# Optimization experiments

Hardware: AMD Instinct MI355X
Metric: run time of the kernel (lower is better)

## Reference

```python
import jax, jax.numpy as jnp
import numpy as np

N_NODES = 100000   # number of graph nodes
N_EDGES = 1600000  # adjacency nnz (avg degree 16)
FEAT_NNZ = 1600000 # sparse feature nnz (~16 per node)
F_IN = 512
F_OUT = 128


def setup_inputs() -> dict:
    key = jax.random.key(0)
    k1, k2, k3, k4, k5, k6 = jax.random.split(key, 6)
    adj_indices = jax.random.randint(k1, (2, N_EDGES), 0, N_NODES, dtype=jnp.int64 if jax.config.jax_enable_x64 else jnp.int32)
    adj_values = jax.random.uniform(k2, (N_EDGES,), dtype=jnp.float32)
    feat_rows = jax.random.randint(k3, (FEAT_NNZ,), 0, N_NODES)
    feat_cols = jax.random.randint(k4, (FEAT_NNZ,), 0, F_IN)
    feat_values = jax.random.uniform(k5, (FEAT_NNZ,), dtype=jnp.float32)
    # xavier_uniform init of the dense weight, as in the torch module
    bound = float(np.sqrt(6.0 / (F_IN + F_OUT)))
    weight = jax.random.uniform(k6, (F_IN, F_OUT), dtype=jnp.float32, minval=-bound, maxval=bound)
    return {
        "adj_indices": adj_indices,
        "adj_values": adj_values,
        "feat_rows": feat_rows,
        "feat_cols": feat_cols,
        "feat_values": feat_values,
        "weight": weight,
        "num_nodes": N_NODES,
    }


def _spmm(rows, cols, vals, num_rows, dense):
    """COO sparse [num_rows, ?] @ dense [?, K] -> [num_rows, K]."""
    msgs = vals[:, None] * dense[cols]          # [nnz, K] gather + scale
    return jax.ops.segment_sum(msgs, rows, num_segments=num_rows)


def reference(adj_indices, adj_values, feat_rows, feat_cols, feat_values, weight, num_nodes):
    # spmm(features, W): sparse [N, F_in] @ [F_in, F_out]
    base_features = _spmm(feat_rows, feat_cols, feat_values, num_nodes, weight)
    # spmm(A_hat, base): sparse [N, N] @ [N, F_out]  -- neighbor aggregation
    out = _spmm(adj_indices[0], adj_indices[1], adj_values, num_nodes, base_features)
    return out
```

## Files before the change

kernel.cpp:

```cpp
#include <hip/hip_runtime.h>
#include <stdint.h>

#define N_NODES 100000
#define F_IN    512
#define F_OUT   128
#define BROWS   128
#define NBKT    ((N_NODES + BROWS - 1) / BROWS)
#define CAP     2560
#define EPB     4096

typedef unsigned short     u16;
typedef unsigned int       u32;
typedef unsigned long long u64;
typedef long long          i64;

__device__ __forceinline__ float b2f(u16 u) {
    union { u32 i; float f; } x; x.i = ((u32)u) << 16; return x.f;
}
__device__ __forceinline__ u16 f2b(float f) {
    u32 i = __float_as_uint(f);
    return (u16)((i + 0x7fffu + ((i >> 16) & 1u)) >> 16);
}
__device__ __forceinline__ float blo(u32 u) { return __uint_as_float(u << 16); }
__device__ __forceinline__ float bhi(u32 u) { return __uint_as_float(u & 0xFFFF0000u); }
__device__ __forceinline__ int ld_idx(const void* p, int i, int w64) {
    return w64 ? (int)((const i64*)p)[i] : ((const int*)p)[i];
}
__device__ __forceinline__ u16 ld_val_bf(const void* p, int i, int f32) {
    return f32 ? f2b(((const float*)p)[i]) : ((const u16*)p)[i];
}

__device__ __forceinline__ void ld_idx4(int* r, const void* p, int g, int w64) {
    if (w64) {
        const i64* q = (const i64*)p + 4 * (size_t)g;
        longlong2 a = *(const longlong2*)q;
        longlong2 b = *(const longlong2*)(q + 2);
        r[0] = (int)a.x; r[1] = (int)a.y; r[2] = (int)b.x; r[3] = (int)b.y;
    } else {
        int4 a = *(const int4*)((const int*)p + 4 * (size_t)g);
        r[0] = a.x; r[1] = a.y; r[2] = a.z; r[3] = a.w;
    }
}
__device__ __forceinline__ void ld_val4(u32* v, const void* p, int g, int f32) {
    if (f32) {
        float4 a = *(const float4*)((const float*)p + 4 * (size_t)g);
        v[0] = f2b(a.x); v[1] = f2b(a.y); v[2] = f2b(a.z); v[3] = f2b(a.w);
    } else {
        ushort4 a = *(const ushort4*)((const u16*)p + 4 * (size_t)g);
        v[0] = a.x; v[1] = a.y; v[2] = a.z; v[3] = a.w;
    }
}

__device__ __forceinline__ void sniff3(const u16* w, const u32* adj, const u32* frows,
                                       int* sf, int t) {
    if (t < 64) {
        u32 e0 = (w[t]      >> 7) & 0xFF;
        u32 e1 = (w[64 + t] >> 7) & 0xFF;
        u64 bad = __ballot((e0 > 0x7B) || (e1 > 0x7B));
        u64 za = __ballot(adj[2 * t + 1] == 0u);
        u64 zf = __ballot(frows[2 * t + 1] == 0u);
        if (t == 0) {
            sf[0] = (bad != 0);
            sf[1] = (__popcll(za) >= 32);
            sf[2] = (__popcll(zf) >= 32);
        }
    }
}

__global__ __launch_bounds__(512, 4) void binF_k(
        const void* __restrict__ frows, const void* __restrict__ fcols,
        const void* __restrict__ fvals, int M,
        const void* __restrict__ adjbase, const u16* __restrict__ weight,
        int* __restrict__ gcurF, u32* __restrict__ fbkt) {
    __shared__ int hist[NBKT];
    __shared__ int hbase[NBKT];
    __shared__ int sf[3];
    int t = threadIdx.x;
    sniff3(weight, (const u32*)adjbase, (const u32*)frows, sf, t);
    for (int i = t; i < NBKT; i += 512) hist[i] = 0;
    __syncthreads();
    int f32 = sf[0], f64 = sf[2];
    int start = blockIdx.x * EPB;
    int end = min(start + EPB, M);
    int r[8]; int c[8]; u32 v[8];
    #pragma unroll
    for (int h = 0; h < 2; ++h) {
        int g = (start >> 2) + t + h * 512;
        int e0 = 4 * g;
        if (e0 + 3 < end) {
            ld_idx4(r + 4 * h, frows, g, f64);
            ld_idx4(c + 4 * h, fcols, g, f64);
            ld_val4(v + 4 * h, fvals, g, f32);
        } else {
            #pragma unroll
            for (int j = 0; j < 4; ++j) {
                int jj = 4 * h + j;
                if (e0 + j < end) {
                    r[jj] = ld_idx(frows, e0 + j, f64);
                    c[jj] = ld_idx(fcols, e0 + j, f64);
                    v[jj] = ld_val_bf(fvals, e0 + j, f32);
                } else r[jj] = -1;
            }
        }
    }
    #pragma unroll
    for (int j = 0; j < 8; ++j) if (r[j] >= 0) atomicAdd(&hist[r[j] >> 7], 1);
    __syncthreads();
    for (int i = t; i < NBKT; i += 512) {
        int h = hist[i];
        hbase[i] = h ? atomicAdd(&gcurF[i], h) : 0;
        hist[i] = 0;
    }
    __syncthreads();
    #pragma unroll
    for (int j = 0; j < 8; ++j) if (r[j] >= 0) {
        int b = r[j] >> 7;
        int pos = hbase[b] + atomicAdd(&hist[b], 1);
        if (pos < CAP)
            fbkt[(size_t)b * CAP + pos] = (v[j] << 16) | ((u32)(r[j] & 127) << 9) | (u32)c[j];
    }
}

union S1Mem {
    struct { int hist[NBKT]; int hbase[NBKT]; } bin;
    struct { u32 csr[CAP]; int hcnt[BROWS]; int roff[BROWS + 1]; int cur[BROWS]; } s1;
};

__global__ __launch_bounds__(512, 4) void binAs1_k(
        const void* __restrict__ adjbase, const void* __restrict__ avals, int E, int nAb,
        const u32* __restrict__ frsn, const u16* __restrict__ weight,
        int* __restrict__ gcurA, u64* __restrict__ abkt,
        const int* __restrict__ cntF, const u32* __restrict__ fbkt,
        const void* __restrict__ W, u16* __restrict__ base) {
    __shared__ S1Mem sm;
    __shared__ int sf[3];
    int t = threadIdx.x;
    sniff3(weight, (const u32*)adjbase, frsn, sf, t);
    if ((int)blockIdx.x < nAb) {
        for (int i = t; i < NBKT; i += 512) sm.bin.hist[i] = 0;
        __syncthreads();
        int f32 = sf[0], a64 = sf[1];
        const void* acols = a64 ? (const void*)((const i64*)adjbase + E)
                                : (const void*)((const int*)adjbase + E);
        int start = blockIdx.x * EPB;
        int end = min(start + EPB, E);
        int r[8]; int c[8]; u32 v[8];
        #pragma unroll
        for (int h = 0; h < 2; ++h) {
            int g = (start >> 2) + t + h * 512;
            int e0 = 4 * g;
            if (e0 + 3 < end) {
                ld_idx4(r + 4 * h, adjbase, g, a64);
                ld_idx4(c + 4 * h, acols, g, a64);
                ld_val4(v + 4 * h, avals, g, f32);
            } else {
                #pragma unroll
                for (int j = 0; j < 4; ++j) {
                    int jj = 4 * h + j;
                    if (e0 + j < end) {
                        r[jj] = ld_idx(adjbase, e0 + j, a64);
                        c[jj] = ld_idx(acols, e0 + j, a64);
                        v[jj] = ld_val_bf(avals, e0 + j, f32);
                    } else r[jj] = -1;
                }
            }
        }
        #pragma unroll
        for (int j = 0; j < 8; ++j) if (r[j] >= 0) atomicAdd(&sm.bin.hist[r[j] >> 7], 1);
        __syncthreads();
        for (int i = t; i < NBKT; i += 512) {
            int h = sm.bin.hist[i];
            sm.bin.hbase[i] = h ? atomicAdd(&gcurA[i], h) : 0;
            sm.bin.hist[i] = 0;
        }
        __syncthreads();
        #pragma unroll
        for (int j = 0; j < 8; ++j) if (r[j] >= 0) {
            int b = r[j] >> 7;
            int pos = sm.bin.hbase[b] + atomicAdd(&sm.bin.hist[b], 1);
            if (pos < CAP)
                abkt[(size_t)b * CAP + pos] =
                    ((u64)v[j] << 24) | ((u64)(r[j] & 127) << 17) | (u64)(u32)c[j];
        }
        return;
    }
    int b = blockIdx.x - nAb;
    int n = cntF[b]; if (n > CAP) n = CAP;
    const u32* ed = fbkt + (size_t)b * CAP;
    if (t < BROWS) sm.s1.hcnt[t] = 0;
    __syncthreads();
    int f32 = sf[0];
    u32 pb[5];
    #pragma unroll
    for (int k = 0; k < 5; ++k) { int i = t + k * 512; pb[k] = (i < n) ? ed[i] : 0u; }
    #pragma unroll
    for (int k = 0; k < 5; ++k) { int i = t + k * 512; if (i < n) atomicAdd(&sm.s1.hcnt[(pb[k] >> 9) & 127], 1); }
    __syncthreads();
    if (t < 64) {
        int h0 = sm.s1.hcnt[2 * t], h1 = sm.s1.hcnt[2 * t + 1];
        int s = h0 + h1, v2 = s;
        #pragma unroll
        for (int off = 1; off < 64; off <<= 1) {
            int u = __shfl_up(v2, off);
            if (t >= off) v2 += u;
        }
        int excl = v2 - s;
        sm.s1.roff[2 * t] = excl;     sm.s1.roff[2 * t + 1] = excl + h0;
        sm.s1.cur[2 * t]  = excl;     sm.s1.cur[2 * t + 1]  = excl + h0;
        if (t == 63) sm.s1.roff[128] = v2;
    }
    __syncthreads();
    #pragma unroll
    for (int k = 0; k < 5; ++k) {
        int i = t + k * 512;
        if (i < n) {
            u32 p = pb[k];
            int pos = atomicAdd(&sm.s1.cur[(p >> 9) & 127], 1);
            sm.s1.csr[pos] = p;
        }
    }
    __syncthreads();
    int wave = t >> 6, lane = t & 63, g16 = lane >> 4, l16 = lane & 15;
    #pragma unroll
    for (int set = 0; set < 4; ++set) {
        int row = set * 32 + wave * 4 + g16;
        int s = sm.s1.roff[row], e = sm.s1.roff[row + 1];
        float a0 = 0.f, a1 = 0.f, a2 = 0.f, a3 = 0.f, a4 = 0.f, a5 = 0.f, a6 = 0.f, a7 = 0.f;
        if (f32) {
            const float* Wf = (const float*)W;
            for (int j0 = s; j0 < e; j0 += 4) {
                u32 p[4]; float4 qa[4], qb[4];
                #pragma unroll
                for (int k = 0; k < 4; ++k) { int jk = j0 + k; p[k] = sm.s1.csr[jk < e ? jk : e - 1]; }
                #pragma unroll
                for (int k = 0; k < 4; ++k) {
                    const float* wp = Wf + (size_t)(p[k] & 0x1FF) * F_OUT + l16 * 8;
                    qa[k] = *(const float4*)wp;
                    qb[k] = *(const float4*)(wp + 4);
                }
                #pragma unroll
                for (int k = 0; k < 4; ++k) {
                    float v = (j0 + k < e) ? b2f((u16)(p[k] >> 16)) : 0.f;
                    a0 += v * qa[k].x; a1 += v * qa[k].y;
                    a2 += v * qa[k].z; a3 += v * qa[k].w;
                    a4 += v * qb[k].x; a5 += v * qb[k].y;
                    a6 += v * qb[k].z; a7 += v * qb[k].w;
                }
            }
        } else {
            const u16* Wb = (const u16*)W;
            for (int j0 = s; j0 < e; j0 += 8) {
                u32 p[8]; uint4 q[8];
                #pragma unroll
                for (int k = 0; k < 8; ++k) { int jk = j0 + k; p[k] = sm.s1.csr[jk < e ? jk : e - 1]; }
                #pragma unroll
                for (int k = 0; k < 8; ++k)
                    q[k] = *(const uint4*)(Wb + (size_t)(p[k] & 0x1FF) * F_OUT + l16 * 8);
                #pragma unroll
                for (int k = 0; k < 8; ++k) {
                    float v = (j0 + k < e) ? b2f((u16)(p[k] >> 16)) : 0.f;
                    a0 += v * blo(q[k].x); a1 += v * bhi(q[k].x);
                    a2 += v * blo(q[k].y); a3 += v * bhi(q[k].y);
                    a4 += v * blo(q[k].z); a5 += v * bhi(q[k].z);
                    a6 += v * blo(q[k].w); a7 += v * bhi(q[k].w);
                }
            }
        }
        int gr = b * BROWS + row;
        if (gr < N_NODES) {
            uint4 o;
            o.x = (u32)f2b(a0) | ((u32)f2b(a1) << 16);
            o.y = (u32)f2b(a2) | ((u32)f2b(a3) << 16);
            o.z = (u32)f2b(a4) | ((u32)f2b(a5) << 16);
            o.w = (u32)f2b(a6) | ((u32)f2b(a7) << 16);
            *(uint4*)(base + (size_t)gr * F_OUT + l16 * 8) = o;
        }
    }
}

__global__ __launch_bounds__(512, 4) void stage2_k(const int* __restrict__ cnt,
        const u64* __restrict__ bkts, const u16* __restrict__ base,
        const void* __restrict__ W, const u32* __restrict__ adjsn,
        const u32* __restrict__ frsn, void* __restrict__ out) {
    __shared__ u64 csr[CAP];
    __shared__ int hcnt[BROWS];
    __shared__ int roff[BROWS + 1];
    __shared__ int cur[BROWS];
    __shared__ int sf[3];
    int t = threadIdx.x;
    sniff3((const u16*)W, adjsn, frsn, sf, t);
    int b = blockIdx.x;
    int n = cnt[b]; if (n > CAP) n = CAP;
    const u64* ed = bkts + (size_t)b * CAP;
    if (t < BROWS) hcnt[t] = 0;
    __syncthreads();
    u64 pb[5];
    #pragma unroll
    for (int k = 0; k < 5; ++k) { int i = t + k * 512; pb[k] = (i < n) ? ed[i] : 0ull; }
    #pragma unroll
    for (int k = 0; k < 5; ++k) { int i = t + k * 512; if (i < n) atomicAdd(&hcnt[(int)((pb[k] >> 17) & 127)], 1); }
    __syncthreads();
    if (t < 64) {
        int h0 = hcnt[2 * t], h1 = hcnt[2 * t + 1];
        int s = h0 + h1, v2 = s;
        #pragma unroll
        for (int off = 1; off < 64; off <<= 1) {
            int u = __shfl_up(v2, off);
            if (t >= off) v2 += u;
        }
        int excl = v2 - s;
        roff[2 * t] = excl;     roff[2 * t + 1] = excl + h0;
        cur[2 * t]  = excl;     cur[2 * t + 1]  = excl + h0;
        if (t == 63) roff[128] = v2;
    }
    __syncthreads();
    #pragma unroll
    for (int k = 0; k < 5; ++k) {
        int i = t + k * 512;
        if (i < n) {
            u64 p = pb[k];
            int pos = atomicAdd(&cur[(int)((p >> 17) & 127)], 1);
            csr[pos] = p;
        }
    }
    __syncthreads();
    int wave = t >> 6, lane = t & 63, g16 = lane >> 4, l16 = lane & 15;
    int f32o = sf[0];
    #pragma unroll
    for (int set = 0; set < 4; ++set) {
        int row = set * 32 + wave * 4 + g16;
        int s = roff[row], e = roff[row + 1];
        float a0 = 0.f, a1 = 0.f, a2 = 0.f, a3 = 0.f, a4 = 0.f, a5 = 0.f, a6 = 0.f, a7 = 0.f;
        for (int j0 = s; j0 < e; j0 += 8) {
            u64 p[8]; uint4 q[8];
            #pragma unroll
            for (int k = 0; k < 8; ++k) { int jk = j0 + k; p[k] = csr[jk < e ? jk : e - 1]; }
            #pragma unroll
            for (int k = 0; k < 8; ++k)
                q[k] = *(const uint4*)(base + (size_t)(u32)(p[k] & 0x1FFFF) * F_OUT + l16 * 8);
            #pragma unroll
            for (int k = 0; k < 8; ++k) {
                float v = (j0 + k < e) ? b2f((u16)(p[k] >> 24)) : 0.f;
                a0 += v * blo(q[k].x); a1 += v * bhi(q[k].x);
                a2 += v * blo(q[k].y); a3 += v * bhi(q[k].y);
                a4 += v * blo(q[k].z); a5 += v * bhi(q[k].z);
                a6 += v * blo(q[k].w); a7 += v * bhi(q[k].w);
            }
        }
        int gr = b * BROWS + row;
        if (gr < N_NODES) {
            if (f32o) {
                float* op = (float*)out + (size_t)gr * F_OUT + l16 * 8;
                float4 o0, o1;
                o0.x = a0; o0.y = a1; o0.z = a2; o0.w = a3;
                o1.x = a4; o1.y = a5; o1.z = a6; o1.w = a7;
                *(float4*)op = o0;
                *(float4*)(op + 4) = o1;
            } else {
                uint4 o;
                o.x = (u32)f2b(a0) | ((u32)f2b(a1) << 16);
                o.y = (u32)f2b(a2) | ((u32)f2b(a3) << 16);
                o.z = (u32)f2b(a4) | ((u32)f2b(a5) << 16);
                o.w = (u32)f2b(a6) | ((u32)f2b(a7) << 16);
                *(uint4*)((u16*)out + (size_t)gr * F_OUT + l16 * 8) = o;
            }
        }
    }
}

extern "C" void kernel_launch(void* const* d_in, const int* in_sizes, int n_in,
                              void* d_out, int out_size, void* d_ws, size_t ws_size,
                              hipStream_t stream) {
    const void* adj_idx   = d_in[0];
    const void* adj_vals  = d_in[1];
    const void* feat_rows = d_in[2];
    const void* feat_cols = d_in[3];
    const void* feat_vals = d_in[4];
    const void* weight    = d_in[5];

    const int E = in_sizes[0] / 2;
    const int M = in_sizes[2];

    char* ws = (char*)d_ws;
    size_t o = 0;
    auto alloc = [&](size_t b) { size_t r = o; o += (b + 255) & ~(size_t)255; return r; };
    int* gcurF = (int*)(ws + alloc((size_t)NBKT * 4));
    int* gcurA = (int*)(ws + alloc((size_t)NBKT * 4));
    size_t cur_end = o;
    u32* fbkt  = (u32*)(ws + alloc((size_t)NBKT * CAP * 4));
    u64* abkt  = (u64*)(ws + alloc((size_t)NBKT * CAP * 8));
    u16* base  = (u16*)(ws + alloc((size_t)N_NODES * F_OUT * 2));
    (void)ws_size;

    const int nFb = (M + EPB - 1) / EPB;
    const int nAb = (E + EPB - 1) / EPB;

    hipMemsetAsync(ws, 0, cur_end, stream);
    binF_k<<<nFb, 512, 0, stream>>>(feat_rows, feat_cols, feat_vals, M,
                                    adj_idx, (const u16*)weight, gcurF, fbkt);
    binAs1_k<<<nAb + NBKT, 512, 0, stream>>>(adj_idx, adj_vals, E, nAb,
                                             (const u32*)feat_rows, (const u16*)weight,
                                             gcurA, abkt, gcurF, fbkt, weight, base);
    stage2_k<<<NBKT, 512, 0, stream>>>(gcurA, abkt, base, weight,
                                       (const u32*)adj_idx, (const u32*)feat_rows, d_out);
}
```

Before: 237.1 us.

## Stream stage-2 neighbor rows into LDS via async global_load_lds double buffering

Replaces the register-batched gather of 8 neighbor rows per iteration in stage2 with a double-buffered pipeline. Each wave issues direct global-to-LDS loads (global_load_lds) two edges at a time, waits on vmcnt, and accumulates from shared memory. The intent is to cut register pressure and overlap the gather latency with compute. It adds a 32KB LDS buffer and lowers launch bounds occupancy from 4 to 2, and the smaller per-step batch reduces memory-level parallelism, which may outweigh the overlap. The trip count is also forced to the max across the 4 row groups in the wave.

```diff
diff --git a/kernel.cpp b/kernel.cpp
--- a/kernel.cpp
+++ b/kernel.cpp
@@ -13,6 +13,9 @@
 typedef unsigned int       u32;
 typedef unsigned long long u64;
 typedef long long          i64;
+
+typedef const __attribute__((address_space(1))) void* gas_t;
+typedef __attribute__((address_space(3))) void*       las_t;
 
 __device__ __forceinline__ float b2f(u16 u) {
     union { u32 i; float f; } x; x.i = ((u32)u) << 16; return x.f;
@@ -278,7 +281,13 @@
     }
 }
 
-__global__ __launch_bounds__(512, 4) void stage2_k(const int* __restrict__ cnt,
+#define S2ACC(V, Q) do { \
+    a0 += (V) * blo((Q).x); a1 += (V) * bhi((Q).x); \
+    a2 += (V) * blo((Q).y); a3 += (V) * bhi((Q).y); \
+    a4 += (V) * blo((Q).z); a5 += (V) * bhi((Q).z); \
+    a6 += (V) * blo((Q).w); a7 += (V) * bhi((Q).w); } while (0)
+
+__global__ __launch_bounds__(512, 2) void stage2_k(const int* __restrict__ cnt,
         const u64* __restrict__ bkts, const u16* __restrict__ base,
         const void* __restrict__ W, const u32* __restrict__ adjsn,
         const u32* __restrict__ frsn, void* __restrict__ out) {
@@ -287,6 +296,7 @@
     __shared__ int roff[BROWS + 1];
     __shared__ int cur[BROWS];
     __shared__ int sf[3];
+    __shared__ u16 sbuf[8][2][1024];
     int t = threadIdx.x;
     sniff3((const u16*)W, adjsn, frsn, sf, t);
     int b = blockIdx.x;
@@ -324,27 +334,62 @@
         }
     }
     __syncthreads();
-    int wave = t >> 6, lane = t & 63, g16 = lane >> 4, l16 = lane & 15;
+    int w = t >> 6, lane = t & 63, g16 = lane >> 4, l16 = lane & 15;
     int f32o = sf[0];
     #pragma unroll
     for (int set = 0; set < 4; ++set) {
-        int row = set * 32 + wave * 4 + g16;
+        int row = set * 32 + w * 4 + g16;
         int s = roff[row], e = roff[row + 1];
         float a0 = 0.f, a1 = 0.f, a2 = 0.f, a3 = 0.f, a4 = 0.f, a5 = 0.f, a6 = 0.f, a7 = 0.f;
-        for (int j0 = s; j0 < e; j0 += 8) {
-            u64 p[8]; uint4 q[8];
+        int trips = (e > s) ? ((e - s + 1) >> 1) : 0;
+        int B = trips;
+        B = max(B, __shfl_xor(B, 16));
+        B = max(B, __shfl_xor(B, 32));
+        if (B > 0) {
+            int fb = (e > s) ? s : 0;
+            u16* h0p = &sbuf[w][0][0];
+            u16* h1p = &sbuf[w][1][0];
+            int issued = 0;
             #pragma unroll
-            for (int k = 0; k < 8; ++k) { int jk = j0 + k; p[k] = csr[jk < e ? jk : e - 1]; }
-            #pragma unroll
-            for (int k = 0; k < 8; ++k)
-                q[k] = *(const uint4*)(base + (size_t)(u32)(p[k] & 0x1FFFF) * F_OUT + l16 * 8);
-            #pragma unroll
-            for (int k = 0; k < 8; ++k) {
-                float v = (j0 + k < e) ? b2f((u16)(p[k] >> 24)) : 0.f;
-                a0 += v * blo(q[k].x); a1 += v * bhi(q[k].x);
-                a2 += v * blo(q[k].y); a3 += v * bhi(q[k].y);
-                a4 += v * blo(q[k].z); a5 += v * bhi(q[k].z);
-                a6 += v * blo(q[k].w); a7 += v * bhi(q[k].w);
+            for (int nb = 0; nb < 2; ++nb) {
+                if (nb < B) {
+                    u16* hp = nb ? h1p : h0p;
+                    #pragma unroll
+                    for (int j = 0; j < 2; ++j) {
+                        int idx = s + nb * 2 + j;
+                        u64 p = csr[idx < e ? idx : fb];
+                        const u16* ga = base + (size_t)(u32)(p & 0x1FFFF) * F_OUT + l16 * 8;
+                        __builtin_amdgcn_global_load_lds((gas_t)ga, (las_t)(hp + j * 512), 16, 0, 0);
+                    }
+                    issued = nb + 1;
+                }
+            }
+            for (int bb = 0; bb < B; ++bb) {
+                if (issued - bb >= 2) { asm volatile("s_waitcnt vmcnt(2)" ::: "memory"); }
+                else                  { asm volatile("s_waitcnt vmcnt(0)" ::: "memory"); }
+                __builtin_amdgcn_sched_barrier(0);
+                u16* hp = (bb & 1) ? h1p : h0p;
+                int i0 = s + bb * 2, i1 = i0 + 1;
+                int c0 = i0 < e ? i0 : fb, c1 = i1 < e ? i1 : fb;
+                float v0 = (i0 < e) ? b2f((u16)(csr[c0] >> 24)) : 0.f;
+                float v1 = (i1 < e) ? b2f((u16)(csr[c1] >> 24)) : 0.f;
+                uint4 q0 = *(const uint4*)(hp + g16 * 128 + l16 * 8);
+                uint4 q1 = *(const uint4*)(hp + 512 + g16 * 128 + l16 * 8);
+                S2ACC(v0, q0);
+                S2ACC(v1, q1);
+                __builtin_amdgcn_sched_barrier(0);
+                if (issued < B) {
+                    int nb = issued;
+                    u16* hp2 = (nb & 1) ? h1p : h0p;
+                    #pragma unroll
+                    for (int j = 0; j < 2; ++j) {
+                        int idx = s + nb * 2 + j;
+                        u64 p = csr[idx < e ? idx : fb];
+                        const u16* ga = base + (size_t)(u32)(p & 0x1FFFF) * F_OUT + l16 * 8;
+                        __builtin_amdgcn_global_load_lds((gas_t)ga, (las_t)(hp2 + j * 512), 16, 0, 0);
+                    }
+                    issued++;
+                }
             }
         }
         int gr = b * BROWS + row;
```

Measured after the change: 255.3 us. 7.7% more time.
